# Performance work log

Hardware: AMD Instinct MI355X
Metric: run time of the kernel (lower is better)

## Reference

```python
import jax, jax.numpy as jnp
import numpy as np

NH, NP, C = 12, 4, 768           # heads, points, d_model
HD = C // NH                      # head dim (deform_ratio=1.0)
SHAPES = np.array([[128, 128], [64, 64], [32, 32]], dtype=np.int64)
LSI = np.array([0, 128 * 128, 128 * 128 + 64 * 64], dtype=np.int64)
L = SHAPES.shape[0]
EPS = 1e-6


def setup_inputs() -> dict:
    key = jax.random.key(0)
    ks = jax.random.split(key, 10)
    N, Lq = 4, 64 * 64
    Lin = int((SHAPES[:, 0] * SHAPES[:, 1]).sum())
    s = 0.02
    return {
        "query": jax.random.normal(ks[0], (N, Lq, C), jnp.float32),
        "reference_points": jax.random.uniform(ks[1], (N, Lq, L, 2), dtype=jnp.float32),
        "feat": jax.random.normal(ks[2], (N, Lin, C), jnp.float32),
        "qnorm_w": jnp.ones((C,), jnp.float32),
        "qnorm_b": jnp.zeros((C,), jnp.float32),
        "fnorm_w": jnp.ones((C,), jnp.float32),
        "fnorm_b": jnp.zeros((C,), jnp.float32),
        "gamma": jnp.full((C,), 0.01, jnp.float32),
        "so_w": s * jax.random.normal(ks[3], (C, NH * L * NP * 2), jnp.float32),
        "so_b": s * jax.random.normal(ks[4], (NH * L * NP * 2,), jnp.float32),
        "aw_w": s * jax.random.normal(ks[5], (C, NH * L * NP), jnp.float32),
        "aw_b": s * jax.random.normal(ks[6], (NH * L * NP,), jnp.float32),
        "vp_w": s * jax.random.normal(ks[7], (C, C), jnp.float32),
        "vp_b": jnp.zeros((C,), jnp.float32),
        "op_w": s * jax.random.normal(ks[8], (C, C), jnp.float32),
        "op_b": jnp.zeros((C,), jnp.float32),
        "spatial_shapes": SHAPES,
        "level_start_index": LSI,
    }


def _ln(x, w, b):
    mu = x.mean(-1, keepdims=True)
    var = ((x - mu) ** 2).mean(-1, keepdims=True)
    return (x - mu) * jax.lax.rsqrt(var + EPS) * w + b


def reference(query, reference_points, feat, qnorm_w, qnorm_b, fnorm_w, fnorm_b,
              gamma, so_w, so_b, aw_w, aw_b, vp_w, vp_b, op_w, op_b,
              spatial_shapes, level_start_index):
    N, Lq, C_ = query.shape
    ss = np.asarray(spatial_shapes)
    lsi = np.asarray(level_start_index)
    q = _ln(query, qnorm_w, qnorm_b)
    f = _ln(feat, fnorm_w, fnorm_b)
    # value projection -> [N, nh, Lin, hd]
    value = (f @ vp_w + vp_b).reshape(N, -1, NH, HD).transpose(0, 2, 1, 3)
    off = (q @ so_w + so_b).reshape(N, Lq, NH, L, NP, 2)
    aw = jax.nn.softmax((q @ aw_w + aw_b).reshape(N, Lq, NH, L * NP), axis=-1)
    aw = aw.reshape(N, Lq, NH, L, NP)
    # offset normalizer is (W, H) per level
    offset_norm = jnp.asarray(ss[:, ::-1].copy(), jnp.float32)
    loc = reference_points[:, :, None, :, None, :] + off / offset_norm[None, None, None, :, None, :]
    out = jnp.zeros((N, Lq, NH, HD), query.dtype)
    for l in range(L):
        H_, W_ = int(ss[l, 0]), int(ss[l, 1])
        st = int(lsi[l])
        v = value[:, :, st:st + H_ * W_, :]                     # [N,nh,HW,hd]
        ll = loc[:, :, :, l].transpose(0, 2, 1, 3, 4).reshape(N, NH, Lq * NP, 2)
        # grid_sample, align_corners=False: map [0,1] -> pixel coords
        px = ll[..., 0] * W_ - 0.5
        py = ll[..., 1] * H_ - 0.5
        x0 = jnp.floor(px)
        y0 = jnp.floor(py)
        tx = px - x0
        ty = py - y0
        x0i = x0.astype(jnp.int32)
        y0i = y0.astype(jnp.int32)
        acc = jnp.zeros((N, NH, Lq * NP, HD), query.dtype)
        for dx, dy, w in ((0, 0, (1 - tx) * (1 - ty)), (1, 0, tx * (1 - ty)),
                          (0, 1, (1 - tx) * ty), (1, 1, tx * ty)):
            xi = x0i + dx
            yi = y0i + dy
            ok = (xi >= 0) & (xi < W_) & (yi >= 0) & (yi < H_)  # zero padding
            idx = jnp.clip(yi, 0, H_ - 1) * W_ + jnp.clip(xi, 0, W_ - 1)
            g = jnp.take_along_axis(v, idx[..., None], axis=2)   # [N,nh,Lq*P,hd]
            acc = acc + g * (w * ok)[..., None]
        samp = acc.reshape(N, NH, Lq, NP, HD)
        out = out + jnp.einsum('nhqpd,nqhp->nqhd', samp, aw[:, :, :, l])
    attn = out.reshape(N, Lq, C_) @ op_w + op_b
    return query + gamma * attn
```

## Files before the change

kernel.cpp:

```cpp
#include <hip/hip_runtime.h>
#include <hip/hip_bf16.h>
#include <stdint.h>

#define NHD   12
#define NPT   4
#define CDIM  768
#define HDIM  64
#define NLVL  3
#define LQ    4096
#define NB    4
#define LIN   21504
#define MQ    (NB*LQ)
#define MF    (NB*LIN)
#define CAT_N 512
#define AW_OFF 288
#define WSCL  16.f

typedef float  f32x4  __attribute__((ext_vector_type(4)));
typedef float  f32x2  __attribute__((ext_vector_type(2)));
typedef float  f32x16 __attribute__((ext_vector_type(16)));
typedef int    i32x8  __attribute__((ext_vector_type(8)));

__device__ __forceinline__ i32x8 mk8(uint4 lo, uint4 hi) {
  i32x8 v;
  v[0] = (int)lo.x; v[1] = (int)lo.y; v[2] = (int)lo.z; v[3] = (int)lo.w;
  v[4] = (int)hi.x; v[5] = (int)hi.y; v[6] = (int)hi.z; v[7] = (int)hi.w;
  return v;
}

__global__ __launch_bounds__(256) void prep_weights(
    const float* __restrict__ vp_w, const float* __restrict__ op_w,
    const float* __restrict__ so_w, const float* __restrict__ aw_w,
    const float* __restrict__ so_b, const float* __restrict__ aw_b,
    char* __restrict__ vp_w8, char* __restrict__ op_w8,
    char* __restrict__ cat_w8, float* __restrict__ cat_bp)
{
  const int b = blockIdx.x;
  if (b == 1536) {
    const int i = threadIdx.x;
#pragma unroll
    for (int it = 0; it < 2; ++it) {
      const int idx = i + it * 256;
      float v = 0.f;
      if (idx < 288) v = so_b[idx];
      else if (idx < 432) v = aw_b[idx - AW_OFF];
      cat_bp[idx] = v;
    }
    return;
  }
  const float* W; char* Wt; int Nsrc, rowoff; float scale;
  int lb;
  if (b < 576)       { W = vp_w; Wt = vp_w8;  Nsrc = 768; rowoff = 0;   scale = 1.f;  lb = b; }
  else if (b < 1152) { W = op_w; Wt = op_w8;  Nsrc = 768; rowoff = 0;   scale = 1.f;  lb = b - 576; }
  else if (b < 1368) { W = so_w; Wt = cat_w8; Nsrc = 288; rowoff = 0;   scale = WSCL; lb = b - 1152; }
  else               { W = aw_w; Wt = cat_w8; Nsrc = 144; rowoff = 288; scale = WSCL; lb = b - 1368; }

  __shared__ float t[32][33];
  const int k0 = (lb % 24) * 32;
  const int n0 = (lb / 24) * 32;
  const int tx = threadIdx.x & 31, ty = threadIdx.x >> 5;
#pragma unroll
  for (int i = ty; i < 32; i += 8) {
    const int n = n0 + tx;
    t[i][tx] = (n < Nsrc) ? W[(size_t)(k0 + i) * Nsrc + n] * scale : 0.f;
  }
  __syncthreads();
#pragma unroll
  for (int i = ty; i < 32; i += 8) {
    const int n = rowoff + n0 + i;
    uint32_t pk = __builtin_amdgcn_cvt_pk_fp8_f32(t[tx][i], 0.f, 0, false);
    Wt[(size_t)n * CDIM + k0 + tx] = (char)(pk & 0xff);
  }
}

__global__ __launch_bounds__(256) void ln_wave(const float* __restrict__ x,
                                               const float* __restrict__ w,
                                               const float* __restrict__ b,
                                               char* __restrict__ y) {
  const int row  = blockIdx.x * 4 + (threadIdx.x >> 6);
  const int lane = threadIdx.x & 63;
  const float4* xr = (const float4*)(x + (size_t)row * CDIM);
  float4 v[3];
  v[0] = xr[lane]; v[1] = xr[lane + 64]; v[2] = xr[lane + 128];
  float s1 = 0.f, s2 = 0.f;
#pragma unroll
  for (int i = 0; i < 3; ++i) {
    s1 += v[i].x + v[i].y + v[i].z + v[i].w;
    s2 += v[i].x*v[i].x + v[i].y*v[i].y + v[i].z*v[i].z + v[i].w*v[i].w;
  }
#pragma unroll
  for (int o = 32; o > 0; o >>= 1) { s1 += __shfl_xor(s1, o); s2 += __shfl_xor(s2, o); }
  const float mu = s1 * (1.f / CDIM);
  const float rs = rsqrtf(s2 * (1.f / CDIM) - mu * mu + 1e-6f);
#pragma unroll
  for (int i = 0; i < 3; ++i) {
    const float4 w4 = ((const float4*)w)[lane + i * 64];
    const float4 b4 = ((const float4*)b)[lane + i * 64];
    const float o0 = (v[i].x - mu) * rs * w4.x + b4.x;
    const float o1 = (v[i].y - mu) * rs * w4.y + b4.y;
    const float o2 = (v[i].z - mu) * rs * w4.z + b4.z;
    const float o3 = (v[i].w - mu) * rs * w4.w + b4.w;
    uint32_t pk = 0;
    pk = __builtin_amdgcn_cvt_pk_fp8_f32(o0, o1, pk, false);
    pk = __builtin_amdgcn_cvt_pk_fp8_f32(o2, o3, pk, true);
    ((uint32_t*)(y + (size_t)row * CDIM))[lane + i * 64] = pk;
  }
}

template<int MODE>
__global__ __launch_bounds__(256, 3) void gemm_mx(
    const char* __restrict__ A, const char* __restrict__ Wt,
    const float* __restrict__ bias, void* __restrict__ Cout,
    int M, int N, int K, int nTN, float oscale,
    const float* __restrict__ resid, const float* __restrict__ gammav)
{
  __shared__ __align__(16) char lds[49152];

  int bid = blockIdx.x;
  const int nwg = gridDim.x;
  if ((nwg & 7) == 0) {
    const int chunk = nwg >> 3;
    bid = (bid & 7) * chunk + (bid >> 3);
  }
  const int mt = bid / nTN, ntl = bid - mt * nTN;
  const int m0 = mt * 128, n0 = ntl * 128;
  const int tid  = threadIdx.x;
  const int lane = tid & 63, wid = tid >> 6;
  const int wm = wid >> 1, wn = wid & 1;
  const int lr31 = lane & 31, lkb = lane >> 5;

  f32x16 acc[2][2] = {};

  auto stage = [&](int kt, int buf, int ab) {
    const char* srcM = ab ? Wt : A;
    const int base0 = ab ? n0 : m0;
    const int k0 = kt * 64;
    char* dst0 = lds + buf * 16384 + ab * 8192;
#pragma unroll
    for (int it = 0; it < 2; ++it) {
      const int i = it * 256 + tid;
      const int r = i >> 2, p = i & 3;
      const int c = p ^ (r & 3);
      const char* src = srcM + (size_t)(base0 + r) * K + k0 + c * 16;
      char* dst = dst0 + (it * 256 + wid * 64) * 16;
      __builtin_amdgcn_global_load_lds(
          (const __attribute__((address_space(1))) uint32_t*)src,
          (__attribute__((address_space(3))) uint32_t*)dst, 16, 0, 0);
    }
  };
  auto rdop = [&](int buf, int ab, int row) -> i32x8 {
    const char* base = lds + buf * 16384 + ab * 8192 + row * 64;
    const int s = row & 3;
    const uint4 lo = *(const uint4*)(base + ((2 * lkb)     ^ s) * 16);
    const uint4 hi = *(const uint4*)(base + ((2 * lkb + 1) ^ s) * 16);
    return mk8(lo, hi);
  };

  const int nk = K >> 6;
  stage(0, 0, 0); stage(0, 0, 1);
  stage(1, 1, 0); stage(1, 1, 1);
  asm volatile("s_waitcnt vmcnt(4)" ::: "memory");
  __builtin_amdgcn_s_barrier();
  asm volatile("" ::: "memory");

  for (int t = 0; t < nk; ++t) {
    const int cur = t % 3;
    const i32x8 a0 = rdop(cur, 0, wm * 64 + lr31);
    const i32x8 a1 = rdop(cur, 0, wm * 64 + 32 + lr31);
    const i32x8 b0 = rdop(cur, 1, wn * 64 + lr31);
    const i32x8 b1 = rdop(cur, 1, wn * 64 + 32 + lr31);
    if (t + 2 < nk) { const int tb = (t + 2) % 3; stage(t + 2, tb, 0); stage(t + 2, tb, 1); }
    __builtin_amdgcn_s_setprio(1);
    acc[0][0] = __builtin_amdgcn_mfma_scale_f32_32x32x64_f8f6f4(
        a0, b0, acc[0][0], 0, 0, 0, 0x7F7F7F7F, 0, 0x7F7F7F7F);
    acc[0][1] = __builtin_amdgcn_mfma_scale_f32_32x32x64_f8f6f4(
        a0, b1, acc[0][1], 0, 0, 0, 0x7F7F7F7F, 0, 0x7F7F7F7F);
    acc[1][0] = __builtin_amdgcn_mfma_scale_f32_32x32x64_f8f6f4(
        a1, b0, acc[1][0], 0, 0, 0, 0x7F7F7F7F, 0, 0x7F7F7F7F);
    acc[1][1] = __builtin_amdgcn_mfma_scale_f32_32x32x64_f8f6f4(
        a1, b1, acc[1][1], 0, 0, 0, 0x7F7F7F7F, 0, 0x7F7F7F7F);
    __builtin_amdgcn_s_setprio(0);
    if (t + 2 < nk)      asm volatile("s_waitcnt vmcnt(4)" ::: "memory");
    else if (t + 1 < nk) asm volatile("s_waitcnt vmcnt(0)" ::: "memory");
    __builtin_amdgcn_s_barrier();
    asm volatile("" ::: "memory");
  }

  if constexpr (MODE == 0) {
    const int head  = (n0 + wn * 64) >> 6;
    const int n_img = (unsigned)m0 / LIN;
    char* plane = (char*)Cout + ((size_t)(n_img * NHD + head) * LIN
                                 + (m0 - n_img * LIN)) * 64;
    float bcol[2];
#pragma unroll
    for (int nt2 = 0; nt2 < 2; ++nt2)
      bcol[nt2] = bias[n0 + wn * 64 + nt2 * 32 + lr31];
    float* my = (float*)(lds + wid * 8704);
#pragma unroll
    for (int mt2 = 0; mt2 < 2; ++mt2) {
#pragma unroll
      for (int nt2 = 0; nt2 < 2; ++nt2)
#pragma unroll
        for (int reg = 0; reg < 16; ++reg) {
          const int row = (reg & 3) + 8 * (reg >> 2) + 4 * lkb;
          my[row * 68 + nt2 * 32 + lr31] = acc[mt2][nt2][reg] + bcol[nt2];
        }
#pragma unroll
      for (int it = 0; it < 2; ++it) {
        const int idx = it * 64 + lane;
        const int row = idx >> 2, seg = idx & 3;
        const float* s = my + row * 68 + seg * 16;
        uint32_t w[4];
#pragma unroll
        for (int q = 0; q < 4; ++q) {
          uint32_t pk = 0;
          pk = __builtin_amdgcn_cvt_pk_fp8_f32(s[q*4+0], s[q*4+1], pk, false);
          pk = __builtin_amdgcn_cvt_pk_fp8_f32(s[q*4+2], s[q*4+3], pk, true);
          w[q] = pk;
        }
        char* orow = plane + (size_t)(wm * 64 + mt2 * 32 + row) * 64 + seg * 16;
        *(uint4*)orow = *(uint4*)w;
      }
    }
  } else {
#pragma unroll
    for (int nt2 = 0; nt2 < 2; ++nt2) {
      const int col = n0 + wn * 64 + nt2 * 32 + lr31;
      const float bcol = bias[col];
      float gcol = 0.f;
      if constexpr (MODE == 2) gcol = gammav[col];
#pragma unroll
      for (int mt2 = 0; mt2 < 2; ++mt2)
#pragma unroll
        for (int reg = 0; reg < 16; ++reg) {
          const int row = m0 + wm * 64 + mt2 * 32
                        + (reg & 3) + 8 * (reg >> 2) + 4 * lkb;
          const size_t o = (size_t)row * N + col;
          if constexpr (MODE == 1)
            ((float*)Cout)[o] = acc[mt2][nt2][reg] * oscale + bcol;
          else
            ((float*)Cout)[o] = resid[o] + gcol * (acc[mt2][nt2][reg] + bcol);
        }
    }
  }
}

__global__ void softmax_pack(const float* __restrict__ raw,
                             const float* __restrict__ refp,
                             float4* __restrict__ params) {
  const int t = blockIdx.x * 256 + threadIdx.x;
  const int h = t % NHD, nq = t / NHD;
  const float* p = raw + (size_t)nq * CAT_N + AW_OFF + h * 12;
  float v[12], m = -1e30f;
#pragma unroll
  for (int j = 0; j < 12; ++j) { v[j] = p[j]; m = fmaxf(m, v[j]); }
  float s = 0.f;
#pragma unroll
  for (int j = 0; j < 12; ++j) { v[j] = __expf(v[j] - m); s += v[j]; }
  const float inv = 1.f / s;
  const float* op = raw + (size_t)nq * CAT_N + h * 24;
  const float* rp = refp + (size_t)nq * (NLVL * 2);
  float4* out = params + (size_t)t * 12;
  const float Wf[3] = {128.f, 64.f, 32.f};
#pragma unroll
  for (int l = 0; l < NLVL; ++l) {
    const float rxw = rp[2 * l] * Wf[l] - 0.5f;
    const float ryw = rp[2 * l + 1] * Wf[l] - 0.5f;
#pragma unroll
    for (int pt = 0; pt < NPT; ++pt) {
      float4 o4;
      o4.x = rxw + op[(l * 4 + pt) * 2 + 0];
      o4.y = ryw + op[(l * 4 + pt) * 2 + 1];
      o4.z = v[l * 4 + pt] * inv;
      o4.w = 0.f;
      out[l * 4 + pt] = o4;
    }
  }
}

__global__ __launch_bounds__(256) void deform_grp16(
    const char* __restrict__ vbytes, const float4* __restrict__ params,
    char* __restrict__ samp)
{
  const int j = blockIdx.x;
  const int x = j & 7, k = j >> 3;
  const int g = x + ((k >> 6) << 3);
  const int i = k & 63;
  const int n = g / NHD, h = g - n * NHD;
  const int wid = threadIdx.x >> 6, lane = threadIdx.x & 63;
  const int qi = lane >> 2, ci = lane & 3;
  const int q  = i * 64 + wid * 16 + qi;
  const int nq = n * LQ + q;
  const float4* __restrict__ pp = params + ((size_t)nq * NHD + h) * 12;
  const uint32_t base0 = (uint32_t)g * (uint32_t)(LIN * 64)
                       + ((uint32_t)ci << 4);

  float acc[16];
#pragma unroll
  for (int c = 0; c < 16; ++c) acc[c] = 0.f;

  const int      Wl[3]  = {128, 64, 32};
  const uint32_t STb[3] = {0u, 16384u * 64u, 20480u * 64u};

#pragma unroll
  for (int l = 0; l < NLVL; ++l) {
    const int W_ = Wl[l];
    const uint32_t base = base0 + STb[l];
#pragma unroll
    for (int p = 0; p < NPT; ++p) {
      const float4 pt = pp[l * 4 + p];
      const float fx = floorf(pt.x), fy = floorf(pt.y);
      const float tx = pt.x - fx,   ty = pt.y - fy;
      const int x0 = (int)fx, y0 = (int)fy;
      const int x1 = x0 + 1,  y1 = y0 + 1;
      const float wx0 = ((uint32_t)x0 < (uint32_t)W_) ? (1.f - tx) : 0.f;
      const float wx1 = ((uint32_t)x1 < (uint32_t)W_) ? tx : 0.f;
      const float wy0 = ((uint32_t)y0 < (uint32_t)W_) ? pt.z * (1.f - ty) : 0.f;
      const float wy1 = ((uint32_t)y1 < (uint32_t)W_) ? pt.z * ty : 0.f;
      const int xc0 = min(max(x0, 0), W_ - 1);
      const int xc1 = min(max(x1, 0), W_ - 1);
      const int yr0 = min(max(y0, 0), W_ - 1) * W_;
      const int yr1 = min(max(y1, 0), W_ - 1) * W_;
      const float cw[4] = {wy0 * wx0, wy0 * wx1, wy1 * wx0, wy1 * wx1};
      const uint4 G0 = *(const uint4*)(vbytes + base + (uint32_t)(yr0 + xc0) * 64u);
      const uint4 G1 = *(const uint4*)(vbytes + base + (uint32_t)(yr0 + xc1) * 64u);
      const uint4 G2 = *(const uint4*)(vbytes + base + (uint32_t)(yr1 + xc0) * 64u);
      const uint4 G3 = *(const uint4*)(vbytes + base + (uint32_t)(yr1 + xc1) * 64u);
      const uint4 GG[4] = {G0, G1, G2, G3};
#pragma unroll
      for (int cnr = 0; cnr < 4; ++cnr) {
        const uint32_t wds[4] = {GG[cnr].x, GG[cnr].y, GG[cnr].z, GG[cnr].w};
        const float wgt = cw[cnr];
#pragma unroll
        for (int wd = 0; wd < 4; ++wd) {
          f32x2 lo = __builtin_amdgcn_cvt_pk_f32_fp8(wds[wd], false);
          f32x2 hi = __builtin_amdgcn_cvt_pk_f32_fp8(wds[wd], true);
          acc[wd * 4 + 0] += lo[0] * wgt;
          acc[wd * 4 + 1] += lo[1] * wgt;
          acc[wd * 4 + 2] += hi[0] * wgt;
          acc[wd * 4 + 3] += hi[1] * wgt;
        }
      }
    }
  }

  uint32_t out[4];
#pragma unroll
  for (int wd = 0; wd < 4; ++wd) {
    uint32_t pk = 0;
    pk = __builtin_amdgcn_cvt_pk_fp8_f32(acc[wd*4+0], acc[wd*4+1], pk, false);
    pk = __builtin_amdgcn_cvt_pk_fp8_f32(acc[wd*4+2], acc[wd*4+3], pk, true);
    out[wd] = pk;
  }
  *(uint4*)(samp + (size_t)nq * CDIM + h * HDIM + ci * 16) = *(uint4*)out;
}

extern "C" void kernel_launch(void* const* d_in, const int* in_sizes, int n_in,
                              void* d_out, int out_size, void* d_ws, size_t ws_size,
                              hipStream_t stream) {
  const float* query = (const float*)d_in[0];
  const float* refp  = (const float*)d_in[1];
  const float* feat  = (const float*)d_in[2];
  const float* qn_w  = (const float*)d_in[3];
  const float* qn_b  = (const float*)d_in[4];
  const float* fn_w  = (const float*)d_in[5];
  const float* fn_b  = (const float*)d_in[6];
  const float* gamma = (const float*)d_in[7];
  const float* so_w  = (const float*)d_in[8];
  const float* so_b  = (const float*)d_in[9];
  const float* aw_w  = (const float*)d_in[10];
  const float* aw_b  = (const float*)d_in[11];
  const float* vp_w  = (const float*)d_in[12];
  const float* vp_b  = (const float*)d_in[13];
  const float* op_w  = (const float*)d_in[14];
  const float* op_b  = (const float*)d_in[15];

  char* ws = (char*)d_ws;
  size_t off = 0;
  auto alloc = [&](size_t bytes) {
    char* p = ws + off;
    off = (off + bytes + 255) & ~(size_t)255;
    return p;
  };
  char*   q_f8   = (char*)alloc((size_t)MQ * CDIM);
  char*   val_f8 = (char*)alloc((size_t)MF * CDIM);
  char*   vp_w8  = (char*)alloc((size_t)CDIM * CDIM);
  char*   op_w8  = (char*)alloc((size_t)CDIM * CDIM);
  char*   cat_w8 = (char*)alloc((size_t)CAT_N * CDIM);
  float*  cat_bp = (float*)alloc(CAT_N * 4);

  const size_t r = off;
  char* f_f8 = ws + r;
  const size_t f_end = r + (size_t)MF * CDIM;
  size_t o2 = r;
  float*  raw     = (float*)(ws + o2);  o2 += (size_t)MQ * CAT_N * 4;
  float4* params  = (float4*)(ws + o2); o2 += (size_t)MQ * NHD * 12 * 16;
  char*   samp8   = (char*)(ws + o2);   o2 += (size_t)MQ * CDIM;
  const size_t need = (f_end > o2) ? f_end : o2;
  if (ws_size < need) return;

  prep_weights<<<1537, 256, 0, stream>>>(vp_w, op_w, so_w, aw_w, so_b, aw_b,
                                         vp_w8, op_w8, cat_w8, cat_bp);

  ln_wave<<<MQ / 4, 256, 0, stream>>>(query, qn_w, qn_b, q_f8);
  ln_wave<<<MF / 4, 256, 0, stream>>>(feat, fn_w, fn_b, f_f8);

  gemm_mx<0><<<(MF / 128) * (CDIM / 128), 256, 0, stream>>>(
      f_f8, vp_w8, vp_b, val_f8, MF, CDIM, CDIM, CDIM / 128,
      1.f, nullptr, nullptr);

  gemm_mx<1><<<(MQ / 128) * (CAT_N / 128), 256, 0, stream>>>(
      q_f8, cat_w8, cat_bp, raw, MQ, CAT_N, CDIM, CAT_N / 128,
      1.f / WSCL, nullptr, nullptr);

  softmax_pack<<<(MQ * NHD) / 256, 256, 0, stream>>>(raw, refp, params);

  deform_grp16<<<48 * 64, 256, 0, stream>>>(val_f8, params, samp8);

  gemm_mx<2><<<(MQ / 128) * (CDIM / 128), 256, 0, stream>>>(
      samp8, op_w8, op_b, (float*)d_out, MQ, CDIM, CDIM, CDIM / 128,
      1.f, query, gamma);
}
```

Baseline: 272.0 us.

## Load GEMM B operand directly from global into registers, stage only A in LDS

The FP8 MFMA GEMM now stages only the A tile through LDS with async global-to-LDS loads. Each wave reads its B (weight) fragments straight from global memory into registers every k-step. This shrinks the LDS footprint and halves the staging traffic through LDS, which may allow more resident workgroups. In exchange, B is fetched per wave with strided row accesses that are shared across waves only through cache. The explicit vmcnt waits for A staging were removed, so A-tile readiness now depends on compiler-inserted waits, which is a synchronisation risk.

Result: slower. 322.6 us (+18.6%).

```diff
diff --git a/kernel.cpp b/kernel.cpp
--- a/kernel.cpp
+++ b/kernel.cpp
@@ -114,7 +114,7 @@
     int M, int N, int K, int nTN, float oscale,
     const float* __restrict__ resid, const float* __restrict__ gammav)
 {
-  __shared__ __align__(16) char lds[49152];
+  __shared__ __align__(16) char lds[36864];
 
   int bid = blockIdx.x;
   const int nwg = gridDim.x;
@@ -131,45 +131,49 @@
 
   f32x16 acc[2][2] = {};
 
-  auto stage = [&](int kt, int buf, int ab) {
-    const char* srcM = ab ? Wt : A;
-    const int base0 = ab ? n0 : m0;
+  auto stageA = [&](int kt, int buf) {
     const int k0 = kt * 64;
-    char* dst0 = lds + buf * 16384 + ab * 8192;
+    char* dst0 = lds + buf * 8192;
 #pragma unroll
     for (int it = 0; it < 2; ++it) {
       const int i = it * 256 + tid;
       const int r = i >> 2, p = i & 3;
       const int c = p ^ (r & 3);
-      const char* src = srcM + (size_t)(base0 + r) * K + k0 + c * 16;
+      const char* src = A + (size_t)(m0 + r) * K + k0 + c * 16;
       char* dst = dst0 + (it * 256 + wid * 64) * 16;
       __builtin_amdgcn_global_load_lds(
           (const __attribute__((address_space(1))) uint32_t*)src,
           (__attribute__((address_space(3))) uint32_t*)dst, 16, 0, 0);
     }
   };
-  auto rdop = [&](int buf, int ab, int row) -> i32x8 {
-    const char* base = lds + buf * 16384 + ab * 8192 + row * 64;
+  auto rdA = [&](int buf, int row) -> i32x8 {
+    const char* base = lds + buf * 8192 + row * 64;
     const int s = row & 3;
     const uint4 lo = *(const uint4*)(base + ((2 * lkb)     ^ s) * 16);
     const uint4 hi = *(const uint4*)(base + ((2 * lkb + 1) ^ s) * 16);
     return mk8(lo, hi);
   };
+  auto rdB = [&](int kt, int nt2) -> i32x8 {
+    const char* p = Wt + (size_t)(n0 + wn * 64 + nt2 * 32 + lr31) * K
+                       + kt * 64 + lkb * 32;
+    const uint4 lo = *(const uint4*)p;
+    const uint4 hi = *(const uint4*)(p + 16);
+    return mk8(lo, hi);
+  };
 
   const int nk = K >> 6;
-  stage(0, 0, 0); stage(0, 0, 1);
-  stage(1, 1, 0); stage(1, 1, 1);
-  asm volatile("s_waitcnt vmcnt(4)" ::: "memory");
+  stageA(0, 0); stageA(1, 1);
+  asm volatile("s_waitcnt vmcnt(2)" ::: "memory");
   __builtin_amdgcn_s_barrier();
   asm volatile("" ::: "memory");
 
   for (int t = 0; t < nk; ++t) {
     const int cur = t % 3;
-    const i32x8 a0 = rdop(cur, 0, wm * 64 + lr31);
-    const i32x8 a1 = rdop(cur, 0, wm * 64 + 32 + lr31);
-    const i32x8 b0 = rdop(cur, 1, wn * 64 + lr31);
-    const i32x8 b1 = rdop(cur, 1, wn * 64 + 32 + lr31);
-    if (t + 2 < nk) { const int tb = (t + 2) % 3; stage(t + 2, tb, 0); stage(t + 2, tb, 1); }
+    const i32x8 b0 = rdB(t, 0);
+    const i32x8 b1 = rdB(t, 1);
+    const i32x8 a0 = rdA(cur, wm * 64 + lr31);
+    const i32x8 a1 = rdA(cur, wm * 64 + 32 + lr31);
+    if (t + 2 < nk) stageA(t + 2, (t + 2) % 3);
     __builtin_amdgcn_s_setprio(1);
     acc[0][0] = __builtin_amdgcn_mfma_scale_f32_32x32x64_f8f6f4(
         a0, b0, acc[0][0], 0, 0, 0, 0x7F7F7F7F, 0, 0x7F7F7F7F);
@@ -180,8 +184,6 @@
     acc[1][1] = __builtin_amdgcn_mfma_scale_f32_32x32x64_f8f6f4(
         a1, b1, acc[1][1], 0, 0, 0, 0x7F7F7F7F, 0, 0x7F7F7F7F);
     __builtin_amdgcn_s_setprio(0);
-    if (t + 2 < nk)      asm volatile("s_waitcnt vmcnt(4)" ::: "memory");
-    else if (t + 1 < nk) asm volatile("s_waitcnt vmcnt(0)" ::: "memory");
     __builtin_amdgcn_s_barrier();
     asm volatile("" ::: "memory");
   }
```
